# Kernel tuning notes

Hardware: AMD Instinct MI355X
Metric: run time of the kernel (lower is better)

Reference implementation:

```python
import jax, jax.numpy as jnp
import numpy as np
from jax import lax

SOS_IDX = 1
EOS_IDX = 2

B, T, K = 32, 256, 128


def setup_inputs() -> dict:
    key = jax.random.key(0)
    k1, k2, k3, k4 = jax.random.split(key, 4)
    h = jax.random.normal(k1, (B, T, K), dtype=jnp.float32)
    transition = jax.random.normal(k2, (K, K), dtype=jnp.float32) * 0.1
    y = jax.random.randint(k3, (B, T), 0, K)
    lengths = jnp.maximum(jax.random.randint(k4, (B,), 1, T + 1), 1)
    mask = jnp.arange(T)[None, :] < lengths[:, None]  # [B, T] bool, contiguous prefix
    return {"h": h, "transition": transition, "y": y, "lengths": lengths, "mask": mask}


def reference(h, transition, y, lengths, mask):
    """CRF negative log-likelihood, same math as CRF.nll."""
    b, t_len, k = h.shape
    # crf_scores[b,t,i,j] = h[b,t,j] + transition[i,j]
    scores = h[:, :, None, :] + transition[None, None, :, :]  # [B,T,K,K]

    # Golden path score: score of transition prev_tag -> tag at each valid step.
    prev_y = jnp.concatenate(
        [jnp.full((b, 1), SOS_IDX, dtype=y.dtype), y[:, :-1]], axis=1
    )  # [B,T]
    gold = jnp.take_along_axis(
        jnp.take_along_axis(scores, prev_y[:, :, None, None], axis=2)[:, :, 0, :],
        y[:, :, None],
        axis=2,
    )[:, :, 0]  # [B,T]
    golden_scores = jnp.sum(jnp.where(mask, gold, jnp.zeros((), h.dtype)))

    # Forward (alpha) recurrence in log space; freeze alpha past sequence end.
    alpha0 = scores[:, 0, SOS_IDX, :]  # [B,K] (all lengths >= 1)
    scores_tbkk = jnp.swapaxes(scores, 0, 1)  # [T,B,K,K]
    mask_tb = jnp.swapaxes(mask, 0, 1)  # [T,B]

    def step(alpha, xs):
        s_t, m_t = xs  # [B,K,K], [B]
        new_alpha = jax.nn.logsumexp(s_t + alpha[:, :, None], axis=1)  # [B,K]
        return jnp.where(m_t[:, None], new_alpha, alpha), None

    alpha, _ = lax.scan(step, alpha0, (scores_tbkk[1:], mask_tb[1:]))
    Z = jnp.sum(alpha[:, EOS_IDX])
    loss = (Z - golden_scores) / b
    return loss
```

## Files before the change

kernel.cpp:

```cpp
#include <hip/hip_runtime.h>
#include <stdint.h>

#define SOS_IDX 1
#define EOS_IDX 2
#define Bb 32
#define Tt 256
#define Kk 128
#define SK 136

typedef unsigned short ushort_t;
typedef __attribute__((ext_vector_type(8))) short short8;
typedef __attribute__((ext_vector_type(4))) float float4v;

__device__ __forceinline__ ushort_t f2bf(float x) {
    union { float f; uint32_t u; } c; c.f = x;
    uint32_t u = c.u + 0x7FFFu + ((c.u >> 16) & 1u);
    return (ushort_t)(u >> 16);
}
__device__ __forceinline__ float bf2f(ushort_t s) {
    union { uint32_t u; float f; } c; c.u = ((uint32_t)s) << 16;
    return c.f;
}
__device__ __forceinline__ float bflo(uint32_t u) {
    union { uint32_t u; float f; } c; c.u = u << 16; return c.f;
}
__device__ __forceinline__ float bfhi(uint32_t u) {
    union { uint32_t u; float f; } c; c.u = u & 0xFFFF0000u; return c.f;
}
__device__ __forceinline__ uint32_t pk2bf(float a, float b) {
    union { float f; uint32_t u; } ca, cb; ca.f = a; cb.f = b;
    uint32_t ua = ca.u + 0x7FFFu + ((ca.u >> 16) & 1u);
    uint32_t ub = cb.u + 0x7FFFu + ((cb.u >> 16) & 1u);
    return __builtin_amdgcn_perm(ub, ua, 0x07060302u);
}

__global__ __launch_bounds__(256, 2) void crf_stageA(const float* __restrict__ h,
                                                     const float* __restrict__ trans,
                                                     const int* __restrict__ lengths,
                                                     ushort_t* __restrict__ Qt,
                                                     float* __restrict__ Ls,
                                                     int NC, int CSPAN) {
    const int st = blockIdx.x, c = blockIdx.y, b = blockIdx.z;
    const int tid = threadIdx.x;
    const int lane = tid & 63, w = tid >> 6;
    const int c15 = lane & 15, q = lane >> 4;
    const int len = lengths[b];
    int ts = c * CSPAN; if (ts < 1) ts = 1;
    int te = (c + 1) * CSPAN; if (te > Tt) te = Tt;
    const int tE = te < len ? te : len;
    if (ts >= tE) return;
    const int nsteps = tE - ts;
    const size_t qoff = ((size_t)b * NC + c) * (Kk * Kk);
    const int nbase = st * 32;

    __shared__ __align__(16) ushort_t s_S[2][32 * SK];
    __shared__ __align__(16) ushort_t s_ehb[32][Kk];
    __shared__ float s_wmax[2][4];

    for (int tl = w; tl < nsteps; tl += 4) {
        const float* hr = &h[((size_t)b * Tt + ts + tl) * Kk];
        s_ehb[tl][lane]      = f2bf(__expf(hr[lane]));
        s_ehb[tl][lane + 64] = f2bf(__expf(hr[lane + 64]));
    }

    short8 afr[2][4];
#pragma unroll
    for (int round = 0; round < 2; ++round) {
        for (int i = 0; i < 32; ++i) {
            int item = i * 256 + tid;
            int m = item & 63, k = item >> 6;
            s_S[m >> 5][(m & 31) * SK + k] = f2bf(__expf(trans[k * Kk + round * 64 + m]));
        }
        __syncthreads();
        if ((w >> 1) == round) {
            const ushort_t* sb = s_S[w & 1];
#pragma unroll
            for (int mt = 0; mt < 2; ++mt)
#pragma unroll
                for (int kt = 0; kt < 4; ++kt)
                    afr[mt][kt] = *(const short8*)&sb[(mt * 16 + c15) * SK + kt * 32 + q * 8];
        }
        __syncthreads();
    }

#pragma unroll
    for (int j = 0; j < 2; ++j) {
        int idx = j * 256 + tid;
        int nl = idx >> 4, oct = idx & 15;
        short8 z = {0, 0, 0, 0, 0, 0, 0, 0};
        int d = nbase + nl - oct * 8;
        if (d >= 0 && d < 8) z[d] = (short)0x3F80;
        *(short8*)&s_S[0][nl * SK + oct * 8] = z;
    }
    __syncthreads();

    float L = 0.0f;
    int cur = 0;
    for (int s = 0; s < nsteps; ++s) {
        float invG = 1.0f;
        if (s > 0 && (s & 3) == 0) {
            int ms = ((s >> 2) - 1) & 1;
            float g = fmaxf(fmaxf(s_wmax[ms][0], s_wmax[ms][1]),
                            fmaxf(s_wmax[ms][2], s_wmax[ms][3]));
            invG = 1.0f / g;
            L += __logf(g);
        }
        const bool isMark = ((s & 3) == 3) || (s == nsteps - 1);

        float sc0[4], sc1[4];
        {
            uint2 u0 = *(const uint2*)&s_ehb[s][w * 32 + q * 4];
            uint2 u1 = *(const uint2*)&s_ehb[s][w * 32 + 16 + q * 4];
            sc0[0] = bflo(u0.x) * invG; sc0[1] = bfhi(u0.x) * invG;
            sc0[2] = bflo(u0.y) * invG; sc0[3] = bfhi(u0.y) * invG;
            sc1[0] = bflo(u1.x) * invG; sc1[1] = bfhi(u1.x) * invG;
            sc1[2] = bflo(u1.y) * invG; sc1[3] = bfhi(u1.y) * invG;
        }

        short8 bfr[2][4];
        const ushort_t* ps = s_S[cur];
#pragma unroll
        for (int nt = 0; nt < 2; ++nt)
#pragma unroll
            for (int kt = 0; kt < 4; ++kt)
                bfr[nt][kt] = *(const short8*)&ps[(nt * 16 + c15) * SK + kt * 32 + q * 8];

        float4v acc[2][2];
#pragma unroll
        for (int mt = 0; mt < 2; ++mt)
#pragma unroll
            for (int nt = 0; nt < 2; ++nt) acc[mt][nt] = (float4v){0.f, 0.f, 0.f, 0.f};
#pragma unroll
        for (int kt = 0; kt < 4; ++kt)
#pragma unroll
            for (int mt = 0; mt < 2; ++mt)
#pragma unroll
                for (int nt = 0; nt < 2; ++nt)
                    acc[mt][nt] = __builtin_amdgcn_mfma_f32_16x16x32_bf16(
                        afr[mt][kt], bfr[nt][kt], acc[mt][nt], 0, 0, 0);

        int nxt = cur ^ 1;
        ushort_t* pn = s_S[nxt];
        float lmax = 0.0f;
#pragma unroll
        for (int mt = 0; mt < 2; ++mt)
#pragma unroll
            for (int nt = 0; nt < 2; ++nt) {
                float v0 = acc[mt][nt][0] * (mt ? sc1[0] : sc0[0]);
                float v1 = acc[mt][nt][1] * (mt ? sc1[1] : sc0[1]);
                float v2 = acc[mt][nt][2] * (mt ? sc1[2] : sc0[2]);
                float v3 = acc[mt][nt][3] * (mt ? sc1[3] : sc0[3]);
                lmax = fmaxf(lmax, fmaxf(fmaxf(v0, v1), fmaxf(v2, v3)));
                uint2 u; u.x = pk2bf(v0, v1); u.y = pk2bf(v2, v3);
                *(uint2*)&pn[(nt * 16 + c15) * SK + w * 32 + mt * 16 + q * 4] = u;
            }
        if (isMark) {
#pragma unroll
            for (int o = 1; o < 64; o <<= 1) lmax = fmaxf(lmax, __shfl_xor(lmax, o));
            if (lane == 0) s_wmax[(s >> 2) & 1][w] = lmax;
        }
        __syncthreads();
        cur = nxt;
    }

    int fs = ((nsteps - 1) >> 2) & 1;
    float Gf = fmaxf(fmaxf(s_wmax[fs][0], s_wmax[fs][1]),
                     fmaxf(s_wmax[fs][2], s_wmax[fs][3]));
    float dsc = 1.0f / Gf;
    L += __logf(Gf);
    const ushort_t* pc = s_S[cur];
#pragma unroll
    for (int j = 0; j < 2; ++j) {
        int idx = j * 256 + tid;
        int n = idx & 127, o = idx >> 7;
        uint4 gv; ushort_t* gp = (ushort_t*)&gv;
#pragma unroll
        for (int r = 0; r < 8; ++r)
            gp[r] = f2bf(bf2f(pc[(o * 8 + r) * SK + n]) * dsc);
        *(uint4*)&Qt[qoff + (size_t)n * Kk + nbase + o * 8] = gv;
    }
    if (tid == 0) Ls[(((size_t)b * NC + c) << 2) + st] = L;
}

__global__ __launch_bounds__(512, 1) void crf_stageB(const float* __restrict__ h,
                                                     const float* __restrict__ trans,
                                                     const int* __restrict__ y,
                                                     const int* __restrict__ lengths,
                                                     const ushort_t* __restrict__ Qt,
                                                     const float* __restrict__ Ls,
                                                     float* __restrict__ out,
                                                     int NC, int CSPAN) {
    const int b = blockIdx.x;
    const int tid = threadIdx.x;
    const int lane = tid & 63, w = tid >> 6;
    const int n = tid >> 2, qr = tid & 3;
    const int len = lengths[b];

    __shared__ __align__(16) float vbuf[2][Kk];
    __shared__ float s_wmax[2][8];
    __shared__ float red[8];
    __shared__ float gred[4];

    if (w < 4) {
        float g = 0.0f;
        if (tid < len) {
            int yt   = y[b * Tt + tid];
            int prev = (tid == 0) ? SOS_IDX : y[b * Tt + tid - 1];
            g = h[((size_t)b * Tt + tid) * Kk + yt] + trans[prev * Kk + yt];
        }
#pragma unroll
        for (int off = 32; off > 0; off >>= 1) g += __shfl_down(g, off);
        if (lane == 0) gred[w] = g;
    }

    float a0 = h[((size_t)b * Tt) * Kk + n] + trans[SOS_IDX * Kk + n];
    float m0 = a0;
#pragma unroll
    for (int o = 1; o < 64; o <<= 1) m0 = fmaxf(m0, __shfl_xor(m0, o));
    if (lane == 0) red[w] = m0;
    __syncthreads();
    {
        float4 r0 = *(const float4*)&red[0];
        float4 r1 = *(const float4*)&red[4];
        m0 = fmaxf(fmaxf(fmaxf(r0.x, r0.y), fmaxf(r0.z, r0.w)),
                   fmaxf(fmaxf(r1.x, r1.y), fmaxf(r1.z, r1.w)));
    }
    float cacc = m0;
    if (qr == 0) vbuf[0][n] = __expf(a0 - m0);

    const int NCR = (len <= 1) ? 0 : min(NC, (len + CSPAN - 1) / CSPAN);
    const size_t lbase = (size_t)b * NC;
    uint4 qb[4];
    if (NCR > 0) {
        const uint4* qp = (const uint4*)(Qt + lbase * (Kk * Kk) + n * Kk + qr * 32);
#pragma unroll
        for (int r = 0; r < 4; ++r) qb[r] = qp[r];
    }
    __syncthreads();
    if (tid == 0)
        atomicAdd(out, -(gred[0] + gred[1] + gred[2] + gred[3]) * (1.0f / (float)Bb));

    int cur = 0;
    for (int ci = 0; ci < NCR; ++ci) {
        uint4 qn[4];
        if (ci + 1 < NCR) {
            const uint4* qp2 = (const uint4*)(Qt + (lbase + ci + 1) * (Kk * Kk) + n * Kk + qr * 32);
#pragma unroll
            for (int r = 0; r < 4; ++r) qn[r] = qp2[r];
        }
        float4 Ls4 = *(const float4*)&Ls[(lbase + ci) << 2];
        float Lref = fmaxf(fmaxf(Ls4.x, Ls4.y), fmaxf(Ls4.z, Ls4.w));
        float lsq = (qr == 0) ? Ls4.x : (qr == 1) ? Ls4.y : (qr == 2) ? Ls4.z : Ls4.w;
        float eQ = __expf(lsq - Lref);
        float invG = 1.0f;
        if (ci > 0 && (ci & 3) == 0) {
            int ms = ((ci >> 2) - 1) & 1;
            float4 r0 = *(const float4*)&s_wmax[ms][0];
            float4 r1 = *(const float4*)&s_wmax[ms][4];
            float g = fmaxf(fmaxf(fmaxf(r0.x, r0.y), fmaxf(r0.z, r0.w)),
                            fmaxf(fmaxf(r1.x, r1.y), fmaxf(r1.z, r1.w)));
            invG = 1.0f / g;
            cacc += __logf(g);
        }
        cacc += Lref;

        float acc0 = 0.0f, acc1 = 0.0f;
#pragma unroll
        for (int r = 0; r < 4; ++r) {
            uint4 d = qb[r];
            float4 v0 = *(const float4*)&vbuf[cur][qr * 32 + r * 8];
            float4 v1 = *(const float4*)&vbuf[cur][qr * 32 + r * 8 + 4];
            acc0 = fmaf(bflo(d.x), v0.x, acc0);
            acc1 = fmaf(bfhi(d.x), v0.y, acc1);
            acc0 = fmaf(bflo(d.y), v0.z, acc0);
            acc1 = fmaf(bfhi(d.y), v0.w, acc1);
            acc0 = fmaf(bflo(d.z), v1.x, acc0);
            acc1 = fmaf(bfhi(d.z), v1.y, acc1);
            acc0 = fmaf(bflo(d.w), v1.z, acc0);
            acc1 = fmaf(bfhi(d.w), v1.w, acc1);
        }
        float s = (acc0 + acc1) * (eQ * invG);
        s += __shfl_xor(s, 1);
        s += __shfl_xor(s, 2);

        const bool isMark = ((ci & 3) == 3) || (ci == NCR - 1);
        if (isMark) {
            float wm = s;
#pragma unroll
            for (int o = 1; o < 64; o <<= 1) wm = fmaxf(wm, __shfl_xor(wm, o));
            if (lane == 0) s_wmax[(ci >> 2) & 1][w] = wm;
        }
        int nxt = cur ^ 1;
        if (qr == 0) vbuf[nxt][n] = s;
        __syncthreads();
        cur = nxt;
        if (ci + 1 < NCR) {
#pragma unroll
            for (int r = 0; r < 4; ++r) qb[r] = qn[r];
        }
    }

    if (tid == 0) {
        atomicAdd(out, (cacc + __logf(vbuf[cur][EOS_IDX])) * (1.0f / (float)Bb));
    }
}

extern "C" void kernel_launch(void* const* d_in, const int* in_sizes, int n_in,
                              void* d_out, int out_size, void* d_ws, size_t ws_size,
                              hipStream_t stream) {
    const float* h       = (const float*)d_in[0];
    const float* trans   = (const float*)d_in[1];
    const int*   y       = (const int*)d_in[2];
    const int*   lengths = (const int*)d_in[3];
    float* out = (float*)d_out;

    int NC = 16;
    while (NC > 8) {
        size_t need = (size_t)Bb * NC * Kk * Kk * 2 + (size_t)Bb * NC * 16;
        if (need <= ws_size) break;
        NC >>= 1;
    }
    int CSPAN = Tt / NC;
    ushort_t* Qt = (ushort_t*)d_ws;
    float* Ls = (float*)((char*)d_ws + (size_t)Bb * NC * Kk * Kk * 2);

    hipMemsetAsync(out, 0, sizeof(float), stream);
    crf_stageA<<<dim3(4, NC, Bb), 256, 0, stream>>>(h, trans, lengths, Qt, Ls, NC, CSPAN);
    crf_stageB<<<Bb, 512, 0, stream>>>(h, trans, y, lengths, Qt, Ls, out, NC, CSPAN);
}
```

Baseline: 115.0 us.

## Precompute exp'd bf16 emissions and transitions in a prep kernel, raise chunk count

```diff
diff --git a/kernel.cpp b/kernel.cpp
--- a/kernel.cpp
+++ b/kernel.cpp
@@ -34,13 +34,41 @@
     return __builtin_amdgcn_perm(ub, ua, 0x07060302u);
 }
 
-__global__ __launch_bounds__(256, 2) void crf_stageA(const float* __restrict__ h,
-                                                     const float* __restrict__ trans,
+__global__ __launch_bounds__(256) void crf_prep(const float* __restrict__ h,
+                                                const float* __restrict__ trans,
+                                                ushort_t* __restrict__ EH,
+                                                ushort_t* __restrict__ ETT) {
+    const int tid = threadIdx.x, bid = blockIdx.x;
+    if (bid < 512) {
+        int base = (bid * 256 + tid) * 8;
+        float4 a = *(const float4*)&h[base];
+        float4 b = *(const float4*)&h[base + 4];
+        uint4 o;
+        o.x = pk2bf(__expf(a.x), __expf(a.y));
+        o.y = pk2bf(__expf(a.z), __expf(a.w));
+        o.z = pk2bf(__expf(b.x), __expf(b.y));
+        o.w = pk2bf(__expf(b.z), __expf(b.w));
+        *(uint4*)&EH[base] = o;
+    } else {
+        int idx = ((bid - 512) * 256 + tid) * 8;
+        int m = idx >> 7, k0 = idx & 127;
+        float e[8];
+#pragma unroll
+        for (int r = 0; r < 8; ++r) e[r] = __expf(trans[(k0 + r) * Kk + m]);
+        uint4 o;
+        o.x = pk2bf(e[0], e[1]); o.y = pk2bf(e[2], e[3]);
+        o.z = pk2bf(e[4], e[5]); o.w = pk2bf(e[6], e[7]);
+        *(uint4*)&ETT[idx] = o;
+    }
+}
+
+__global__ __launch_bounds__(256, 4) void crf_stageA(const ushort_t* __restrict__ EH,
+                                                     const ushort_t* __restrict__ ETT,
                                                      const int* __restrict__ lengths,
                                                      ushort_t* __restrict__ Qt,
                                                      float* __restrict__ Ls,
                                                      int NC, int CSPAN) {
-    const int st = blockIdx.x, c = blockIdx.y, b = blockIdx.z;
+    const int st = blockIdx.x, b = blockIdx.y, c = blockIdx.z;
     const int tid = threadIdx.x;
     const int lane = tid & 63, w = tid >> 6;
     const int c15 = lane & 15, q = lane >> 4;
@@ -54,34 +82,14 @@
     const int nbase = st * 32;
 
     __shared__ __align__(16) ushort_t s_S[2][32 * SK];
-    __shared__ __align__(16) ushort_t s_ehb[32][Kk];
     __shared__ float s_wmax[2][4];
 
-    for (int tl = w; tl < nsteps; tl += 4) {
-        const float* hr = &h[((size_t)b * Tt + ts + tl) * Kk];
-        s_ehb[tl][lane]      = f2bf(__expf(hr[lane]));
-        s_ehb[tl][lane + 64] = f2bf(__expf(hr[lane + 64]));
-    }
-
     short8 afr[2][4];
 #pragma unroll
-    for (int round = 0; round < 2; ++round) {
-        for (int i = 0; i < 32; ++i) {
-            int item = i * 256 + tid;
-            int m = item & 63, k = item >> 6;
-            s_S[m >> 5][(m & 31) * SK + k] = f2bf(__expf(trans[k * Kk + round * 64 + m]));
-        }
-        __syncthreads();
-        if ((w >> 1) == round) {
-            const ushort_t* sb = s_S[w & 1];
-#pragma unroll
-            for (int mt = 0; mt < 2; ++mt)
-#pragma unroll
-                for (int kt = 0; kt < 4; ++kt)
-                    afr[mt][kt] = *(const short8*)&sb[(mt * 16 + c15) * SK + kt * 32 + q * 8];
-        }
-        __syncthreads();
-    }
+    for (int mt = 0; mt < 2; ++mt)
+#pragma unroll
+        for (int kt = 0; kt < 4; ++kt)
+            afr[mt][kt] = *(const short8*)&ETT[(w * 32 + mt * 16 + c15) * Kk + kt * 32 + q * 8];
 
 #pragma unroll
     for (int j = 0; j < 2; ++j) {
@@ -92,11 +100,20 @@
         if (d >= 0 && d < 8) z[d] = (short)0x3F80;
         *(short8*)&s_S[0][nl * SK + oct * 8] = z;
     }
+
+    const ushort_t* ehb = EH + ((size_t)b * Tt) * Kk;
+    uint2 hp0 = *(const uint2*)&ehb[(size_t)ts * Kk + w * 32 + q * 4];
+    uint2 hp1 = *(const uint2*)&ehb[(size_t)ts * Kk + w * 32 + 16 + q * 4];
     __syncthreads();
 
     float L = 0.0f;
     int cur = 0;
     for (int s = 0; s < nsteps; ++s) {
+        uint2 e0 = hp0, e1 = hp1;
+        if (s + 1 < nsteps) {
+            hp0 = *(const uint2*)&ehb[(size_t)(ts + s + 1) * Kk + w * 32 + q * 4];
+            hp1 = *(const uint2*)&ehb[(size_t)(ts + s + 1) * Kk + w * 32 + 16 + q * 4];
+        }
         float invG = 1.0f;
         if (s > 0 && (s & 3) == 0) {
             int ms = ((s >> 2) - 1) & 1;
@@ -108,14 +125,10 @@
         const bool isMark = ((s & 3) == 3) || (s == nsteps - 1);
 
         float sc0[4], sc1[4];
-        {
-            uint2 u0 = *(const uint2*)&s_ehb[s][w * 32 + q * 4];
-            uint2 u1 = *(const uint2*)&s_ehb[s][w * 32 + 16 + q * 4];
-            sc0[0] = bflo(u0.x) * invG; sc0[1] = bfhi(u0.x) * invG;
-            sc0[2] = bflo(u0.y) * invG; sc0[3] = bfhi(u0.y) * invG;
-            sc1[0] = bflo(u1.x) * invG; sc1[1] = bfhi(u1.x) * invG;
-            sc1[2] = bflo(u1.y) * invG; sc1[3] = bfhi(u1.y) * invG;
-        }
+        sc0[0] = bflo(e0.x) * invG; sc0[1] = bfhi(e0.x) * invG;
+        sc0[2] = bflo(e0.y) * invG; sc0[3] = bfhi(e0.y) * invG;
+        sc1[0] = bflo(e1.x) * invG; sc1[1] = bfhi(e1.x) * invG;
+        sc1[2] = bflo(e1.y) * invG; sc1[3] = bfhi(e1.y) * invG;
 
         short8 bfr[2][4];
         const ushort_t* ps = s_S[cur];
@@ -314,17 +327,23 @@
     const int*   lengths = (const int*)d_in[3];
     float* out = (float*)d_out;
 
-    int NC = 16;
+    const size_t ehBytes  = (size_t)Bb * Tt * Kk * 2;
+    const size_t ettBytes = (size_t)Kk * Kk * 2;
+    int NC = 32;
     while (NC > 8) {
-        size_t need = (size_t)Bb * NC * Kk * Kk * 2 + (size_t)Bb * NC * 16;
+        size_t need = (size_t)Bb * NC * Kk * Kk * 2 + ehBytes + ettBytes
+                    + (size_t)Bb * NC * 16;
         if (need <= ws_size) break;
         NC >>= 1;
     }
     int CSPAN = Tt / NC;
-    ushort_t* Qt = (ushort_t*)d_ws;
-    float* Ls = (float*)((char*)d_ws + (size_t)Bb * NC * Kk * Kk * 2);
+    ushort_t* Qt  = (ushort_t*)d_ws;
+    ushort_t* EH  = (ushort_t*)((char*)d_ws + (size_t)Bb * NC * Kk * Kk * 2);
+    ushort_t* ETT = EH + (size_t)Bb * Tt * Kk;
+    float*    Ls  = (float*)(ETT + Kk * Kk);
 
     hipMemsetAsync(out, 0, sizeof(float), stream);
-    crf_stageA<<<dim3(4, NC, Bb), 256, 0, stream>>>(h, trans, lengths, Qt, Ls, NC, CSPAN);
+    crf_prep<<<520, 256, 0, stream>>>(h, trans, EH, ETT);
+    crf_stageA<<<dim3(4, Bb, NC), 256, 0, stream>>>(EH, ETT, lengths, Qt, Ls, NC, CSPAN);
     crf_stageB<<<Bb, 512, 0, stream>>>(h, trans, y, lengths, Qt, Ls, out, NC, CSPAN);
 }
```

Result: slower. 130.8 us (+13.8%).
